# Kernel tuning notes

Hardware: AMD Instinct MI355X
Metric: run time of the kernel (lower is better)

The kernel has to match this reference:

```python
import jax, jax.numpy as jnp
import numpy as np

N_NODES = 100000
IN_CH, HID_CH, OUT_CH = 128, 128, 64
N_EDGES = 1600000


def _gcn_conv(x, W, b, src, dst, num_nodes):
    """PyG GCNConv with gcn_norm(add_self_loops=True): adds one self-loop per
    node to the given edge set, symmetric deg^-1/2 normalization, then
    gather-scale-scatter of the linearly transformed features."""
    loop = jnp.arange(num_nodes)
    s = jnp.concatenate([src, loop])
    d = jnp.concatenate([dst, loop])
    # degree over targets (flow source_to_target), edge weights = 1
    deg = jax.ops.segment_sum(jnp.ones_like(s, x.dtype), d, num_segments=num_nodes)
    dinv = jnp.where(deg > 0, deg ** -0.5, 0.0)
    norm = dinv[s] * dinv[d]                      # [E']
    h = x @ W                                     # [N, out]
    msg = h[s] * norm[:, None]                    # [E', out] gather + scale
    out = jax.ops.segment_sum(msg, d, num_segments=num_nodes)  # scatter-add
    return out + b


def setup_inputs() -> dict:
    key = jax.random.key(0)
    k = jax.random.split(key, 6)
    x = jax.random.normal(k[0], (N_NODES, IN_CH), dtype=jnp.float32)
    edge_index = jax.random.randint(k[1], (2, N_EDGES), 0, N_NODES, dtype=jnp.int64)
    # Glorot-scale params
    W1 = jax.random.normal(k[2], (IN_CH, HID_CH), dtype=jnp.float32) * (2.0 / (IN_CH + HID_CH)) ** 0.5
    b1 = jnp.zeros((HID_CH,), dtype=jnp.float32)
    W2 = jax.random.normal(k[3], (HID_CH, OUT_CH), dtype=jnp.float32) * (2.0 / (HID_CH + OUT_CH)) ** 0.5
    b2 = jnp.zeros((OUT_CH,), dtype=jnp.float32)
    return {"x": x, "edge_index": edge_index, "W1": W1, "b1": b1, "W2": W2, "b2": b2}


def reference(x, edge_index, W1, b1, W2, b2):
    num_nodes = x.shape[0]
    loop = jnp.arange(num_nodes, dtype=edge_index.dtype)
    # wrapper-level add_self_loops (GCNConv adds another internally)
    src = jnp.concatenate([edge_index[0], loop])
    dst = jnp.concatenate([edge_index[1], loop])
    h = _gcn_conv(x, W1, b1, src, dst, num_nodes)
    h = jax.nn.relu(h)
    h = _gcn_conv(h, W2, b2, src, dst, num_nodes)
    return jax.nn.log_softmax(h, axis=1)
```

## Files before the change

### kernel.cpp

```cpp
#include <hip/hip_runtime.h>
#include <cstdint>
#include <cstddef>

#define IN_CH 128
#define HID_CH 128
#define OUT_CH 64
#define BSH 8
#define PB 4096

typedef unsigned int uint32;
typedef unsigned char uchar;
typedef short bf16x8 __attribute__((ext_vector_type(8)));
typedef float f32x4 __attribute__((ext_vector_type(4)));
typedef float f32x2 __attribute__((ext_vector_type(2)));

static __device__ __forceinline__ unsigned short f2bf(float f) {
    uint32 u = __float_as_uint(f);
    u += 0x7fffu + ((u >> 16) & 1u);
    return (unsigned short)(u >> 16);
}
static __device__ __forceinline__ uchar f2fp8(float f) {
    int p = __builtin_amdgcn_cvt_pk_fp8_f32(f, f, 0, false);
    return (uchar)(p & 0xff);
}


__global__ __launch_bounds__(256) void bhist_wtrans(
    const int* __restrict__ dst, int* __restrict__ bcnt, int E, int NB, int gP,
    const float* __restrict__ W1, const float* __restrict__ W2,
    unsigned short* __restrict__ W1t, unsigned short* __restrict__ W2t) {
    if (blockIdx.x >= (uint32)gP) {
        int t = (blockIdx.x - gP) * 256 + threadIdx.x;
        if (t < 128 * 128) {
            int nc = t >> 7, k = t & 127;
            W1t[t] = f2bf(W1[k * 128 + nc]);
        }
        int u = t - 128 * 128;
        if (u >= 0 && u < 64 * 128) {
            int nc = u >> 7, k = u & 127;
            W2t[u] = f2bf(W2[k * 64 + nc]);
        }
        return;
    }
    __shared__ int h[512];
    int t = threadIdx.x;
    int e0 = blockIdx.x * PB;
    int cnt = min(PB, E - e0);
    for (int b = t; b < NB; b += 256) h[b] = 0;
    __syncthreads();
    for (int i = t; i < cnt; i += 256)
        atomicAdd(&h[dst[e0 + i] >> BSH], 1);
    __syncthreads();
    for (int b = t; b < NB; b += 256)
        if (h[b]) atomicAdd(&bcnt[b], h[b]);
}

__global__ void bscan(const int* __restrict__ bcnt, int* __restrict__ bbase,
                      int* __restrict__ bcur, int NB, int E) {
    __shared__ int s[512];
    int t = threadIdx.x;
    int v = (t < NB) ? bcnt[t] : 0;
    s[t] = v;
    __syncthreads();
    for (int o = 1; o < 512; o <<= 1) {
        int add = (t >= o) ? s[t - o] : 0;
        __syncthreads();
        s[t] += add;
        __syncthreads();
    }
    if (t < NB) { bbase[t] = s[t] - v; bcur[t] = 0; }
    if (t == 0) bbase[NB] = E;
}

__global__ __launch_bounds__(256) void part1(
    const int* __restrict__ src, const int* __restrict__ dst,
    const int* __restrict__ bbase, int* __restrict__ bcur,
    int2* __restrict__ pairBuf, int E, int NB) {
    __shared__ int2 pairs[PB];
    __shared__ int hist[512];
    __shared__ int base[512];
    int t = threadIdx.x;
    int e0 = blockIdx.x * PB;
    int cnt = min(PB, E - e0);
    for (int b = t; b < NB; b += 256) hist[b] = 0;
    __syncthreads();
    for (int i = t; i < cnt; i += 256) {
        int s = src[e0 + i], d = dst[e0 + i];
        pairs[i] = make_int2(s, d);
        atomicAdd(&hist[d >> BSH], 1);
    }
    __syncthreads();
    for (int b = t; b < NB; b += 256) {
        int h = hist[b];
        int gb = (h > 0) ? atomicAdd(&bcur[b], h) : 0;
        base[b] = bbase[b] + gb;
        hist[b] = 0;
    }
    __syncthreads();
    for (int i = t; i < cnt; i += 256) {
        int2 p = pairs[i];
        int b = p.y >> BSH;
        int q = base[b] + atomicAdd(&hist[b], 1);
        pairBuf[q] = p;
    }
}

__global__ __launch_bounds__(256) void bucket_build(
    const int2* __restrict__ pairBuf, const int* __restrict__ bbase,
    int* __restrict__ rowptr, int* __restrict__ deg, float* __restrict__ dinv,
    int* __restrict__ csr, int N) {
    __shared__ int cnt[256];
    __shared__ int loc[256];
    int b = blockIdx.x, t = threadIdx.x;
    int start = bbase[b], end = bbase[b + 1];
    cnt[t] = 0;
    __syncthreads();
    for (int i = start + t; i < end; i += 256)
        atomicAdd(&cnt[pairBuf[i].y & 255], 1);
    __syncthreads();
    int v = cnt[t];
    loc[t] = v;
    __syncthreads();
    for (int o = 1; o < 256; o <<= 1) {
        int add = (t >= o) ? loc[t - o] : 0;
        __syncthreads();
        loc[t] += add;
        __syncthreads();
    }
    int excl = loc[t] - v;
    int node = (b << BSH) + t;
    if (node < N) {
        rowptr[node] = start + excl;
        deg[node] = v;
        dinv[node] = rsqrtf((float)(v + 2));
    }
    __syncthreads();
    cnt[t] = excl;
    __syncthreads();
    for (int i = start + t; i < end; i += 256) {
        int2 p = pairBuf[i];
        int q = start + atomicAdd(&cnt[p.y & 255], 1);
        csr[q] = p.x;
    }
}


template <int OUT, bool AFP32>
__global__ __launch_bounds__(256) void gemm_mfma(
    const void* __restrict__ Av, const unsigned short* __restrict__ Wt,
    uchar* __restrict__ C, int n) {
    constexpr int AP = 72;
    constexpr int WP = 136;
    constexpr int NT = OUT / 16;
    __shared__ unsigned short As[128 * AP];
    __shared__ unsigned short Ws[OUT * WP];

    const int t = threadIdx.x;
    const int row0 = blockIdx.x * 128;

    for (int i = t; i < OUT * 16; i += 256) {
        int rr = i >> 4, sq = i & 15;
        *(uint4*)&Ws[rr * WP + sq * 8] = *(const uint4*)(Wt + rr * 128 + sq * 8);
    }

    const int w = t >> 6, l = t & 63;
    const int q = l >> 4, r16 = l & 15;
    const int mbase = w * 32;

    f32x4 acc0[NT], acc1[NT];
    for (int i = 0; i < NT; i++) {
        acc0[i] = (f32x4){0.f, 0.f, 0.f, 0.f};
        acc1[i] = (f32x4){0.f, 0.f, 0.f, 0.f};
    }

    for (int half = 0; half < 2; half++) {
        if (half) __syncthreads();
        if (AFP32) {
            const float* A = (const float*)Av;
            for (int i = t; i < 128 * 16; i += 256) {
                int rr = i >> 4, fq = i & 15;
                float4 v = make_float4(0.f, 0.f, 0.f, 0.f);
                if (row0 + rr < n)
                    v = *(const float4*)(A + (size_t)(row0 + rr) * 128 + half * 64 + fq * 4);
                unsigned short* p = &As[rr * AP + fq * 4];
                p[0] = f2bf(v.x); p[1] = f2bf(v.y); p[2] = f2bf(v.z); p[3] = f2bf(v.w);
            }
        } else {
            const unsigned short* A = (const unsigned short*)Av;
            for (int i = t; i < 128 * 8; i += 256) {
                int rr = i >> 3, sq = i & 7;
                uint4 v = make_uint4(0, 0, 0, 0);
                if (row0 + rr < n)
                    v = *(const uint4*)(A + (size_t)(row0 + rr) * 128 + half * 64 + sq * 8);
                *(uint4*)&As[rr * AP + sq * 8] = v;
            }
        }
        __syncthreads();

#pragma unroll
        for (int kc = 0; kc < 2; kc++) {
            int ko = kc * 32 + q * 8;
            int kow = half * 64 + ko;
            bf16x8 a0 = *(const bf16x8*)&As[(mbase + r16) * AP + ko];
            bf16x8 a1 = *(const bf16x8*)&As[(mbase + 16 + r16) * AP + ko];
#pragma unroll
            for (int nt = 0; nt < NT; nt++) {
                bf16x8 b = *(const bf16x8*)&Ws[(nt * 16 + r16) * WP + kow];
                acc0[nt] = __builtin_amdgcn_mfma_f32_16x16x32_bf16(a0, b, acc0[nt], 0, 0, 0);
                acc1[nt] = __builtin_amdgcn_mfma_f32_16x16x32_bf16(a1, b, acc1[nt], 0, 0, 0);
            }
        }
    }

#pragma unroll
    for (int nt = 0; nt < NT; nt++) {
#pragma unroll
        for (int p = 0; p < 4; p++) {
            int rr = row0 + mbase + q * 4 + p;
            if (rr < n) C[(size_t)rr * OUT + nt * 16 + r16] = f2fp8(acc0[nt][p]);
            if (rr + 16 < n) C[(size_t)(rr + 16) * OUT + nt * 16 + r16] = f2fp8(acc1[nt][p]);
        }
    }
}


__global__ __launch_bounds__(256) void agg_relu_128(
    const uchar* __restrict__ H, const int* __restrict__ csr,
    const int* __restrict__ rowptr, const int* __restrict__ deg,
    const float* __restrict__ dinv, const float* __restrict__ bias,
    unsigned short* __restrict__ out, int n) {
    int v = blockIdx.x * 16 + (threadIdx.x >> 4);
    int hl = threadIdx.x & 15;
    int gsel = threadIdx.x & 48;
    bool valid = v < n;
    int vc = valid ? v : 0;
    int base = rowptr[vc];
    int cnt = valid ? deg[vc] : 0;

    float4 aL0 = make_float4(0.f, 0.f, 0.f, 0.f), aH0 = aL0;
    float4 aL1 = aL0, aH1 = aL0, aL2 = aL0, aH2 = aL0, aL3 = aL0, aH3 = aL0;

    for (int j0 = 0; j0 < cnt; j0 += 16) {
        int nj = min(16, cnt - j0);
        int ul = 0; float wl = 0.f;
        if (hl < nj) { ul = csr[base + j0 + hl]; wl = dinv[ul]; }
        int j = 0;
        for (; j + 4 <= nj; j += 4) {
            int s0 = j | gsel, s1 = (j + 1) | gsel, s2 = (j + 2) | gsel, s3 = (j + 3) | gsel;
            int u0 = __shfl(ul, s0), u1 = __shfl(ul, s1);
            int u2 = __shfl(ul, s2), u3 = __shfl(ul, s3);
            float w0 = __shfl(wl, s0), w1 = __shfl(wl, s1);
            float w2 = __shfl(wl, s2), w3 = __shfl(wl, s3);
            uint2 h0 = *(const uint2*)(H + (size_t)u0 * 128 + hl * 8);
            uint2 h1 = *(const uint2*)(H + (size_t)u1 * 128 + hl * 8);
            uint2 h2 = *(const uint2*)(H + (size_t)u2 * 128 + hl * 8);
            uint2 h3 = *(const uint2*)(H + (size_t)u3 * 128 + hl * 8);
            {
                f32x2 p0 = __builtin_amdgcn_cvt_pk_f32_fp8(h0.x, false);
                f32x2 p1 = __builtin_amdgcn_cvt_pk_f32_fp8(h0.x, true);
                f32x2 p2 = __builtin_amdgcn_cvt_pk_f32_fp8(h0.y, false);
                f32x2 p3 = __builtin_amdgcn_cvt_pk_f32_fp8(h0.y, true);
                aL0.x += w0 * p0[0]; aL0.y += w0 * p0[1]; aL0.z += w0 * p1[0]; aL0.w += w0 * p1[1];
                aH0.x += w0 * p2[0]; aH0.y += w0 * p2[1]; aH0.z += w0 * p3[0]; aH0.w += w0 * p3[1];
            }
            {
                f32x2 p0 = __builtin_amdgcn_cvt_pk_f32_fp8(h1.x, false);
                f32x2 p1 = __builtin_amdgcn_cvt_pk_f32_fp8(h1.x, true);
                f32x2 p2 = __builtin_amdgcn_cvt_pk_f32_fp8(h1.y, false);
                f32x2 p3 = __builtin_amdgcn_cvt_pk_f32_fp8(h1.y, true);
                aL1.x += w1 * p0[0]; aL1.y += w1 * p0[1]; aL1.z += w1 * p1[0]; aL1.w += w1 * p1[1];
                aH1.x += w1 * p2[0]; aH1.y += w1 * p2[1]; aH1.z += w1 * p3[0]; aH1.w += w1 * p3[1];
            }
            {
                f32x2 p0 = __builtin_amdgcn_cvt_pk_f32_fp8(h2.x, false);
                f32x2 p1 = __builtin_amdgcn_cvt_pk_f32_fp8(h2.x, true);
                f32x2 p2 = __builtin_amdgcn_cvt_pk_f32_fp8(h2.y, false);
                f32x2 p3 = __builtin_amdgcn_cvt_pk_f32_fp8(h2.y, true);
                aL2.x += w2 * p0[0]; aL2.y += w2 * p0[1]; aL2.z += w2 * p1[0]; aL2.w += w2 * p1[1];
                aH2.x += w2 * p2[0]; aH2.y += w2 * p2[1]; aH2.z += w2 * p3[0]; aH2.w += w2 * p3[1];
            }
            {
                f32x2 p0 = __builtin_amdgcn_cvt_pk_f32_fp8(h3.x, false);
                f32x2 p1 = __builtin_amdgcn_cvt_pk_f32_fp8(h3.x, true);
                f32x2 p2 = __builtin_amdgcn_cvt_pk_f32_fp8(h3.y, false);
                f32x2 p3 = __builtin_amdgcn_cvt_pk_f32_fp8(h3.y, true);
                aL3.x += w3 * p0[0]; aL3.y += w3 * p0[1]; aL3.z += w3 * p1[0]; aL3.w += w3 * p1[1];
                aH3.x += w3 * p2[0]; aH3.y += w3 * p2[1]; aH3.z += w3 * p3[0]; aH3.w += w3 * p3[1];
            }
        }
        for (; j < nj; j++) {
            int s = j | gsel;
            int u = __shfl(ul, s);
            float wv = __shfl(wl, s);
            uint2 h = *(const uint2*)(H + (size_t)u * 128 + hl * 8);
            f32x2 p0 = __builtin_amdgcn_cvt_pk_f32_fp8(h.x, false);
            f32x2 p1 = __builtin_amdgcn_cvt_pk_f32_fp8(h.x, true);
            f32x2 p2 = __builtin_amdgcn_cvt_pk_f32_fp8(h.y, false);
            f32x2 p3 = __builtin_amdgcn_cvt_pk_f32_fp8(h.y, true);
            aL0.x += wv * p0[0]; aL0.y += wv * p0[1]; aL0.z += wv * p1[0]; aL0.w += wv * p1[1];
            aH0.x += wv * p2[0]; aH0.y += wv * p2[1]; aH0.z += wv * p3[0]; aH0.w += wv * p3[1];
        }
    }
    if (valid) {
        float4 aL = make_float4((aL0.x + aL1.x) + (aL2.x + aL3.x),
                                (aL0.y + aL1.y) + (aL2.y + aL3.y),
                                (aL0.z + aL1.z) + (aL2.z + aL3.z),
                                (aL0.w + aL1.w) + (aL2.w + aL3.w));
        float4 aH = make_float4((aH0.x + aH1.x) + (aH2.x + aH3.x),
                                (aH0.y + aH1.y) + (aH2.y + aH3.y),
                                (aH0.z + aH1.z) + (aH2.z + aH3.z),
                                (aH0.w + aH1.w) + (aH2.w + aH3.w));
        float dv = dinv[vc];
        float sl = 2.f * dv * dv;
        uint2 hv = *(const uint2*)(H + (size_t)vc * 128 + hl * 8);
        f32x2 s0 = __builtin_amdgcn_cvt_pk_f32_fp8(hv.x, false);
        f32x2 s1 = __builtin_amdgcn_cvt_pk_f32_fp8(hv.x, true);
        f32x2 s2 = __builtin_amdgcn_cvt_pk_f32_fp8(hv.y, false);
        f32x2 s3 = __builtin_amdgcn_cvt_pk_f32_fp8(hv.y, true);
        const float4* bp = (const float4*)(bias + hl * 8);
        float4 b0 = bp[0], b1 = bp[1];
        float o0 = fmaxf(dv * aL.x + sl * s0[0] + b0.x, 0.f);
        float o1 = fmaxf(dv * aL.y + sl * s0[1] + b0.y, 0.f);
        float o2 = fmaxf(dv * aL.z + sl * s1[0] + b0.z, 0.f);
        float o3 = fmaxf(dv * aL.w + sl * s1[1] + b0.w, 0.f);
        float o4 = fmaxf(dv * aH.x + sl * s2[0] + b1.x, 0.f);
        float o5 = fmaxf(dv * aH.y + sl * s2[1] + b1.y, 0.f);
        float o6 = fmaxf(dv * aH.z + sl * s3[0] + b1.z, 0.f);
        float o7 = fmaxf(dv * aH.w + sl * s3[1] + b1.w, 0.f);
        uint4 pk;
        pk.x = (uint32)f2bf(o0) | ((uint32)f2bf(o1) << 16);
        pk.y = (uint32)f2bf(o2) | ((uint32)f2bf(o3) << 16);
        pk.z = (uint32)f2bf(o4) | ((uint32)f2bf(o5) << 16);
        pk.w = (uint32)f2bf(o6) | ((uint32)f2bf(o7) << 16);
        *(uint4*)(out + (size_t)vc * 128 + hl * 8) = pk;
    }
}

__global__ __launch_bounds__(256) void agg_lsm_64(
    const uchar* __restrict__ H, const int* __restrict__ csr,
    const int* __restrict__ rowptr, const int* __restrict__ deg,
    const float* __restrict__ dinv, const float* __restrict__ bias,
    float* __restrict__ out, int n) {
    int v = blockIdx.x * 16 + (threadIdx.x >> 4);
    int hl = threadIdx.x & 15;
    int gsel = threadIdx.x & 48;
    bool valid = v < n;
    int vc = valid ? v : 0;
    int base = rowptr[vc];
    int cnt = valid ? deg[vc] : 0;

    float4 a0 = make_float4(0.f, 0.f, 0.f, 0.f), a1 = a0, a2 = a0, a3 = a0;
    for (int j0 = 0; j0 < cnt; j0 += 16) {
        int nj = min(16, cnt - j0);
        int ul = 0; float wl = 0.f;
        if (hl < nj) { ul = csr[base + j0 + hl]; wl = dinv[ul]; }
        int j = 0;
        for (; j + 4 <= nj; j += 4) {
            int s0 = j | gsel, s1 = (j + 1) | gsel, s2 = (j + 2) | gsel, s3 = (j + 3) | gsel;
            int u0 = __shfl(ul, s0), u1 = __shfl(ul, s1);
            int u2 = __shfl(ul, s2), u3 = __shfl(ul, s3);
            float w0 = __shfl(wl, s0), w1 = __shfl(wl, s1);
            float w2 = __shfl(wl, s2), w3 = __shfl(wl, s3);
            uint32 h0 = *(const uint32*)(H + (size_t)u0 * 64 + hl * 4);
            uint32 h1 = *(const uint32*)(H + (size_t)u1 * 64 + hl * 4);
            uint32 h2 = *(const uint32*)(H + (size_t)u2 * 64 + hl * 4);
            uint32 h3 = *(const uint32*)(H + (size_t)u3 * 64 + hl * 4);
            f32x2 l0 = __builtin_amdgcn_cvt_pk_f32_fp8(h0, false);
            f32x2 g0 = __builtin_amdgcn_cvt_pk_f32_fp8(h0, true);
            f32x2 l1 = __builtin_amdgcn_cvt_pk_f32_fp8(h1, false);
            f32x2 g1 = __builtin_amdgcn_cvt_pk_f32_fp8(h1, true);
            f32x2 l2 = __builtin_amdgcn_cvt_pk_f32_fp8(h2, false);
            f32x2 g2 = __builtin_amdgcn_cvt_pk_f32_fp8(h2, true);
            f32x2 l3 = __builtin_amdgcn_cvt_pk_f32_fp8(h3, false);
            f32x2 g3 = __builtin_amdgcn_cvt_pk_f32_fp8(h3, true);
            a0.x += w0 * l0[0]; a0.y += w0 * l0[1]; a0.z += w0 * g0[0]; a0.w += w0 * g0[1];
            a1.x += w1 * l1[0]; a1.y += w1 * l1[1]; a1.z += w1 * g1[0]; a1.w += w1 * g1[1];
            a2.x += w2 * l2[0]; a2.y += w2 * l2[1]; a2.z += w2 * g2[0]; a2.w += w2 * g2[1];
            a3.x += w3 * l3[0]; a3.y += w3 * l3[1]; a3.z += w3 * g3[0]; a3.w += w3 * g3[1];
        }
        for (; j < nj; j++) {
            int s = j | gsel;
            int u = __shfl(ul, s);
            float wv = __shfl(wl, s);
            uint32 h = *(const uint32*)(H + (size_t)u * 64 + hl * 4);
            f32x2 lo = __builtin_amdgcn_cvt_pk_f32_fp8(h, false);
            f32x2 gg = __builtin_amdgcn_cvt_pk_f32_fp8(h, true);
            a0.x += wv * lo[0]; a0.y += wv * lo[1]; a0.z += wv * gg[0]; a0.w += wv * gg[1];
        }
    }
    float4 acc = make_float4((a0.x + a1.x) + (a2.x + a3.x),
                             (a0.y + a1.y) + (a2.y + a3.y),
                             (a0.z + a1.z) + (a2.z + a3.z),
                             (a0.w + a1.w) + (a2.w + a3.w));
    float dv = dinv[vc];
    uint32 hv = *(const uint32*)(H + (size_t)vc * 64 + hl * 4);
    f32x2 dl = __builtin_amdgcn_cvt_pk_f32_fp8(hv, false);
    f32x2 dh = __builtin_amdgcn_cvt_pk_f32_fp8(hv, true);
    float4 bb = ((const float4*)bias)[hl];
    float sl = 2.f * dv * dv;
    float v0 = dv * acc.x + sl * dl[0] + bb.x;
    float v1 = dv * acc.y + sl * dl[1] + bb.y;
    float v2 = dv * acc.z + sl * dh[0] + bb.z;
    float v3 = dv * acc.w + sl * dh[1] + bb.w;
    float m = fmaxf(fmaxf(v0, v1), fmaxf(v2, v3));
    for (int o = 8; o > 0; o >>= 1) m = fmaxf(m, __shfl_xor(m, o));
    float e = (__expf(v0 - m) + __expf(v1 - m)) + (__expf(v2 - m) + __expf(v3 - m));
    for (int o = 8; o > 0; o >>= 1) e += __shfl_xor(e, o);
    float ls = m + __logf(e);
    if (valid)
        *(float4*)(out + (size_t)vc * 64 + hl * 4) =
            make_float4(v0 - ls, v1 - ls, v2 - ls, v3 - ls);
}


extern "C" void kernel_launch(void* const* d_in, const int* in_sizes, int n_in,
                              void* d_out, int out_size, void* d_ws, size_t ws_size,
                              hipStream_t stream) {
    const float* x  = (const float*)d_in[0];
    const int*   ei = (const int*)d_in[1];
    const float* W1 = (const float*)d_in[2];
    const float* b1 = (const float*)d_in[3];
    const float* W2 = (const float*)d_in[4];
    const float* b2 = (const float*)d_in[5];
    float* out = (float*)d_out;

    const int N = in_sizes[0] / IN_CH;
    const int E = in_sizes[1] / 2;
    const int* src = ei;
    const int* dst = ei + E;
    const int NB = (N + 255) >> BSH;

    char* w = (char*)d_ws;
    size_t off = 0;
    auto alloc = [&](size_t bytes) -> char* {
        char* p = w + off;
        off = (off + bytes + 255) & ~(size_t)255;
        return p;
    };
    int*   deg    = (int*)alloc((size_t)N * 4);
    int*   rowptr = (int*)alloc((size_t)N * 4);
    int*   bcnt   = (int*)alloc(512 * 4);
    int*   bbase  = (int*)alloc(513 * 4);
    int*   bcur   = (int*)alloc(512 * 4);
    float* dinv   = (float*)alloc((size_t)N * 4);
    int*   csr    = (int*)alloc((size_t)E * 4);
    unsigned short* W1t = (unsigned short*)alloc(128 * 128 * 2);
    unsigned short* W2t = (unsigned short*)alloc(64 * 128 * 2);
    uchar* H1  = (uchar*)alloc((size_t)N * HID_CH);
    unsigned short* A1b = (unsigned short*)alloc((size_t)N * HID_CH * 2);
    uchar* H2  = H1;
    int2*  pairBuf = (int2*)A1b;

    hipMemsetAsync(bcnt, 0, 512 * 4, stream);

    int gP = (E + PB - 1) / PB;

    bhist_wtrans<<<gP + 96, 256, 0, stream>>>(dst, bcnt, E, NB, gP, W1, W2, W1t, W2t);
    bscan<<<1, 512, 0, stream>>>(bcnt, bbase, bcur, NB, E);
    part1<<<gP, 256, 0, stream>>>(src, dst, bbase, bcur, pairBuf, E, NB);
    bucket_build<<<NB, 256, 0, stream>>>(pairBuf, bbase, rowptr, deg, dinv, csr, N);

    gemm_mfma<128, true><<<(N + 127) / 128, 256, 0, stream>>>(x, W1t, H1, N);
    agg_relu_128<<<(N + 15) / 16, 256, 0, stream>>>(H1, csr, rowptr, deg, dinv, b1, A1b, N);
    gemm_mfma<64, false><<<(N + 127) / 128, 256, 0, stream>>>(A1b, W2t, H2, N);
    agg_lsm_64<<<(N + 15) / 16, 256, 0, stream>>>(H2, csr, rowptr, deg, dinv, b2, out, N);
}
```

Baseline: 252.9 us.

## Fuse edge partition with first GEMM and vectorize aggregation accumulators

Merges the edge-partition kernel and the first MFMA GEMM into one launch, where the first blocks do the partition and the later blocks do GEMM tiles. The two independent phases can then run concurrently, and one launch plus a serialization point are removed. The shared memory is unioned at 53 KB, which may lower occupancy for the partition blocks. The aggregation kernels also switch to packed f32x2 accumulators, aiming for packed FMA instructions.

Result: no change. 253.0 us (+0.1%).

```diff
diff --git a/kernel.cpp b/kernel.cpp
--- a/kernel.cpp
+++ b/kernel.cpp
@@ -72,91 +72,15 @@
     if (t == 0) bbase[NB] = E;
 }
 
-__global__ __launch_bounds__(256) void part1(
-    const int* __restrict__ src, const int* __restrict__ dst,
-    const int* __restrict__ bbase, int* __restrict__ bcur,
-    int2* __restrict__ pairBuf, int E, int NB) {
-    __shared__ int2 pairs[PB];
-    __shared__ int hist[512];
-    __shared__ int base[512];
-    int t = threadIdx.x;
-    int e0 = blockIdx.x * PB;
-    int cnt = min(PB, E - e0);
-    for (int b = t; b < NB; b += 256) hist[b] = 0;
-    __syncthreads();
-    for (int i = t; i < cnt; i += 256) {
-        int s = src[e0 + i], d = dst[e0 + i];
-        pairs[i] = make_int2(s, d);
-        atomicAdd(&hist[d >> BSH], 1);
-    }
-    __syncthreads();
-    for (int b = t; b < NB; b += 256) {
-        int h = hist[b];
-        int gb = (h > 0) ? atomicAdd(&bcur[b], h) : 0;
-        base[b] = bbase[b] + gb;
-        hist[b] = 0;
-    }
-    __syncthreads();
-    for (int i = t; i < cnt; i += 256) {
-        int2 p = pairs[i];
-        int b = p.y >> BSH;
-        int q = base[b] + atomicAdd(&hist[b], 1);
-        pairBuf[q] = p;
-    }
-}
-
-__global__ __launch_bounds__(256) void bucket_build(
-    const int2* __restrict__ pairBuf, const int* __restrict__ bbase,
-    int* __restrict__ rowptr, int* __restrict__ deg, float* __restrict__ dinv,
-    int* __restrict__ csr, int N) {
-    __shared__ int cnt[256];
-    __shared__ int loc[256];
-    int b = blockIdx.x, t = threadIdx.x;
-    int start = bbase[b], end = bbase[b + 1];
-    cnt[t] = 0;
-    __syncthreads();
-    for (int i = start + t; i < end; i += 256)
-        atomicAdd(&cnt[pairBuf[i].y & 255], 1);
-    __syncthreads();
-    int v = cnt[t];
-    loc[t] = v;
-    __syncthreads();
-    for (int o = 1; o < 256; o <<= 1) {
-        int add = (t >= o) ? loc[t - o] : 0;
-        __syncthreads();
-        loc[t] += add;
-        __syncthreads();
-    }
-    int excl = loc[t] - v;
-    int node = (b << BSH) + t;
-    if (node < N) {
-        rowptr[node] = start + excl;
-        deg[node] = v;
-        dinv[node] = rsqrtf((float)(v + 2));
-    }
-    __syncthreads();
-    cnt[t] = excl;
-    __syncthreads();
-    for (int i = start + t; i < end; i += 256) {
-        int2 p = pairBuf[i];
-        int q = start + atomicAdd(&cnt[p.y & 255], 1);
-        csr[q] = p.x;
-    }
-}
-
 
 template <int OUT, bool AFP32>
-__global__ __launch_bounds__(256) void gemm_mfma(
+static __device__ __forceinline__ void gemm_body(
+    unsigned short* As, unsigned short* Ws,
     const void* __restrict__ Av, const unsigned short* __restrict__ Wt,
-    uchar* __restrict__ C, int n) {
+    uchar* __restrict__ C, int n, int row0, int t) {
     constexpr int AP = 72;
     constexpr int WP = 136;
     constexpr int NT = OUT / 16;
-    __shared__ unsigned short As[128 * AP];
-    __shared__ unsigned short Ws[OUT * WP];
-
-    const int t = threadIdx.x;
-    const int row0 = blockIdx.x * 128;
 
     for (int i = t; i < OUT * 16; i += 256) {
         int rr = i >> 4, sq = i & 15;
@@ -223,6 +147,98 @@
     }
 }
 
+__global__ __launch_bounds__(256) void part1_gemm1(
+    const int* __restrict__ src, const int* __restrict__ dst,
+    const int* __restrict__ bbase, int* __restrict__ bcur,
+    int2* __restrict__ pairBuf, int E, int NB, int gP,
+    const float* __restrict__ x, const unsigned short* __restrict__ W1t,
+    uchar* __restrict__ H1, int n) {
+    __shared__ __align__(16) char smem[53248];
+    int t = threadIdx.x;
+
+    if ((int)blockIdx.x >= gP) {
+        unsigned short* As = (unsigned short*)smem;
+        unsigned short* Ws = (unsigned short*)(smem + 18432);
+        gemm_body<128, true>(As, Ws, x, W1t, H1, n, ((int)blockIdx.x - gP) * 128, t);
+        return;
+    }
+
+    int2* pairs = (int2*)smem;
+    int*  hist  = (int*)(smem + 32768);
+    int*  base  = (int*)(smem + 32768 + 2048);
+    int e0 = blockIdx.x * PB;
+    int cnt = min(PB, E - e0);
+    for (int b = t; b < NB; b += 256) hist[b] = 0;
+    __syncthreads();
+    for (int i = t; i < cnt; i += 256) {
+        int s = src[e0 + i], d = dst[e0 + i];
+        pairs[i] = make_int2(s, d);
+        atomicAdd(&hist[d >> BSH], 1);
+    }
+    __syncthreads();
+    for (int b = t; b < NB; b += 256) {
+        int h = hist[b];
+        int gb = (h > 0) ? atomicAdd(&bcur[b], h) : 0;
+        base[b] = bbase[b] + gb;
+        hist[b] = 0;
+    }
+    __syncthreads();
+    for (int i = t; i < cnt; i += 256) {
+        int2 p = pairs[i];
+        int b = p.y >> BSH;
+        int q = base[b] + atomicAdd(&hist[b], 1);
+        pairBuf[q] = p;
+    }
+}
+
+__global__ __launch_bounds__(256) void bucket_build(
+    const int2* __restrict__ pairBuf, const int* __restrict__ bbase,
+    int* __restrict__ rowptr, int* __restrict__ deg, float* __restrict__ dinv,
+    int* __restrict__ csr, int N) {
+    __shared__ int cnt[256];
+    __shared__ int loc[256];
+    int b = blockIdx.x, t = threadIdx.x;
+    int start = bbase[b], end = bbase[b + 1];
+    cnt[t] = 0;
+    __syncthreads();
+    for (int i = start + t; i < end; i += 256)
+        atomicAdd(&cnt[pairBuf[i].y & 255], 1);
+    __syncthreads();
+    int v = cnt[t];
+    loc[t] = v;
+    __syncthreads();
+    for (int o = 1; o < 256; o <<= 1) {
+        int add = (t >= o) ? loc[t - o] : 0;
+        __syncthreads();
+        loc[t] += add;
+        __syncthreads();
+    }
+    int excl = loc[t] - v;
+    int node = (b << BSH) + t;
+    if (node < N) {
+        rowptr[node] = start + excl;
+        deg[node] = v;
+        dinv[node] = rsqrtf((float)(v + 2));
+    }
+    __syncthreads();
+    cnt[t] = excl;
+    __syncthreads();
+    for (int i = start + t; i < end; i += 256) {
+        int2 p = pairBuf[i];
+        int q = start + atomicAdd(&cnt[p.y & 255], 1);
+        csr[q] = p.x;
+    }
+}
+
+template <int OUT, bool AFP32>
+__global__ __launch_bounds__(256) void gemm_mfma(
+    const void* __restrict__ Av, const unsigned short* __restrict__ Wt,
+    uchar* __restrict__ C, int n) {
+    __shared__ unsigned short As[128 * 72];
+    __shared__ unsigned short Ws[OUT * 136];
+    gemm_body<OUT, AFP32>(As, Ws, Av, Wt, C, n, blockIdx.x * 128, threadIdx.x);
+}
+
 
 __global__ __launch_bounds__(256) void agg_relu_128(
     const uchar* __restrict__ H, const int* __restrict__ csr,
@@ -237,8 +253,11 @@
     int base = rowptr[vc];
     int cnt = valid ? deg[vc] : 0;
 
-    float4 aL0 = make_float4(0.f, 0.f, 0.f, 0.f), aH0 = aL0;
-    float4 aL1 = aL0, aH1 = aL0, aL2 = aL0, aH2 = aL0, aL3 = aL0, aH3 = aL0;
+    f32x2 acc[4][4];
+#pragma unroll
+    for (int i = 0; i < 4; i++)
+#pragma unroll
+        for (int p = 0; p < 4; p++) acc[i][p] = (f32x2){0.f, 0.f};
 
     for (int j0 = 0; j0 < cnt; j0 += 16) {
         int nj = min(16, cnt - j0);
@@ -255,61 +274,45 @@
             uint2 h1 = *(const uint2*)(H + (size_t)u1 * 128 + hl * 8);
             uint2 h2 = *(const uint2*)(H + (size_t)u2 * 128 + hl * 8);
             uint2 h3 = *(const uint2*)(H + (size_t)u3 * 128 + hl * 8);
-            {
-                f32x2 p0 = __builtin_amdgcn_cvt_pk_f32_fp8(h0.x, false);
-                f32x2 p1 = __builtin_amdgcn_cvt_pk_f32_fp8(h0.x, true);
-                f32x2 p2 = __builtin_amdgcn_cvt_pk_f32_fp8(h0.y, false);
-                f32x2 p3 = __builtin_amdgcn_cvt_pk_f32_fp8(h0.y, true);
-                aL0.x += w0 * p0[0]; aL0.y += w0 * p0[1]; aL0.z += w0 * p1[0]; aL0.w += w0 * p1[1];
-                aH0.x += w0 * p2[0]; aH0.y += w0 * p2[1]; aH0.z += w0 * p3[0]; aH0.w += w0 * p3[1];
-            }
-            {
-                f32x2 p0 = __builtin_amdgcn_cvt_pk_f32_fp8(h1.x, false);
-                f32x2 p1 = __builtin_amdgcn_cvt_pk_f32_fp8(h1.x, true);
-                f32x2 p2 = __builtin_amdgcn_cvt_pk_f32_fp8(h1.y, false);
-                f32x2 p3 = __builtin_amdgcn_cvt_pk_f32_fp8(h1.y, true);
-                aL1.x += w1 * p0[0]; aL1.y += w1 * p0[1]; aL1.z += w1 * p1[0]; aL1.w += w1 * p1[1];
-                aH1.x += w1 * p2[0]; aH1.y += w1 * p2[1]; aH1.z += w1 * p3[0]; aH1.w += w1 * p3[1];
-            }
-            {
-                f32x2 p0 = __builtin_amdgcn_cvt_pk_f32_fp8(h2.x, false);
-                f32x2 p1 = __builtin_amdgcn_cvt_pk_f32_fp8(h2.x, true);
-                f32x2 p2 = __builtin_amdgcn_cvt_pk_f32_fp8(h2.y, false);
-                f32x2 p3 = __builtin_amdgcn_cvt_pk_f32_fp8(h2.y, true);
-                aL2.x += w2 * p0[0]; aL2.y += w2 * p0[1]; aL2.z += w2 * p1[0]; aL2.w += w2 * p1[1];
-                aH2.x += w2 * p2[0]; aH2.y += w2 * p2[1]; aH2.z += w2 * p3[0]; aH2.w += w2 * p3[1];
-            }
-            {
-                f32x2 p0 = __builtin_amdgcn_cvt_pk_f32_fp8(h3.x, false);
-                f32x2 p1 = __builtin_amdgcn_cvt_pk_f32_fp8(h3.x, true);
-                f32x2 p2 = __builtin_amdgcn_cvt_pk_f32_fp8(h3.y, false);
-                f32x2 p3 = __builtin_amdgcn_cvt_pk_f32_fp8(h3.y, true);
-                aL3.x += w3 * p0[0]; aL3.y += w3 * p0[1]; aL3.z += w3 * p1[0]; aL3.w += w3 * p1[1];
-                aH3.x += w3 * p2[0]; aH3.y += w3 * p2[1]; aH3.z += w3 * p3[0]; aH3.w += w3 * p3[1];
-            }
+            f32x2 wv;
+            wv = (f32x2){w0, w0};
+            acc[0][0] += wv * __builtin_amdgcn_cvt_pk_f32_fp8(h0.x, false);
+            acc[0][1] += wv * __builtin_amdgcn_cvt_pk_f32_fp8(h0.x, true);
+            acc[0][2] += wv * __builtin_amdgcn_cvt_pk_f32_fp8(h0.y, false);
+            acc[0][3] += wv * __builtin_amdgcn_cvt_pk_f32_fp8(h0.y, true);
+            wv = (f32x2){w1, w1};
+            acc[1][0] += wv * __builtin_amdgcn_cvt_pk_f32_fp8(h1.x, false);
+            acc[1][1] += wv * __builtin_amdgcn_cvt_pk_f32_fp8(h1.x, true);
+            acc[1][2] += wv * __builtin_amdgcn_cvt_pk_f32_fp8(h1.y, false);
+            acc[1][3] += wv * __builtin_amdgcn_cvt_pk_f32_fp8(h1.y, true);
+            wv = (f32x2){w2, w2};
+            acc[2][0] += wv * __builtin_amdgcn_cvt_pk_f32_fp8(h2.x, false);
+            acc[2][1] += wv * __builtin_amdgcn_cvt_pk_f32_fp8(h2.x, true);
+            acc[2][2] += wv * __builtin_amdgcn_cvt_pk_f32_fp8(h2.y, false);
+            acc[2][3] += wv * __builtin_amdgcn_cvt_pk_f32_fp8(h2.y, true);
+            wv = (f32x2){w3, w3};
+            acc[3][0] += wv * __builtin_amdgcn_cvt_pk_f32_fp8(h3.x, false);
+            acc[3][1] += wv * __builtin_amdgcn_cvt_pk_f32_fp8(h3.x, true);
+            acc[3][2] += wv * __builtin_amdgcn_cvt_pk_f32_fp8(h3.y, false);
+            acc[3][3] += wv * __builtin_amdgcn_cvt_pk_f32_fp8(h3.y, true);
         }
         for (; j < nj; j++) {
             int s = j | gsel;
             int u = __shfl(ul, s);
-            float wv = __shfl(wl, s);
+            float wf = __shfl(wl, s);
             uint2 h = *(const uint2*)(H + (size_t)u * 128 + hl * 8);
-            f32x2 p0 = __builtin_amdgcn_cvt_pk_f32_fp8(h.x, false);
-            f32x2 p1 = __builtin_amdgcn_cvt_pk_f32_fp8(h.x, true);
-            f32x2 p2 = __builtin_amdgcn_cvt_pk_f32_fp8(h.y, false);
-            f32x2 p3 = __builtin_amdgcn_cvt_pk_f32_fp8(h.y, true);
-            aL0.x += wv * p0[0]; aL0.y += wv * p0[1]; aL0.z += wv * p1[0]; aL0.w += wv * p1[1];
-            aH0.x += wv * p2[0]; aH0.y += wv * p2[1]; aH0.z += wv * p3[0]; aH0.w += wv * p3[1];
+            f32x2 wv = (f32x2){wf, wf};
+            acc[0][0] += wv * __builtin_amdgcn_cvt_pk_f32_fp8(h.x, false);
+            acc[0][1] += wv * __builtin_amdgcn_cvt_pk_f32_fp8(h.x, true);
+            acc[0][2] += wv * __builtin_amdgcn_cvt_pk_f32_fp8(h.y, false);
+            acc[0][3] += wv * __builtin_amdgcn_cvt_pk_f32_fp8(h.y, true);
         }
     }
     if (valid) {
-        float4 aL = make_float4((aL0.x + aL1.x) + (aL2.x + aL3.x),
-                                (aL0.y + aL1.y) + (aL2.y + aL3.y),
-                                (aL0.z + aL1.z) + (aL2.z + aL3.z),
-                                (aL0.w + aL1.w) + (aL2.w + aL3.w));
-        float4 aH = make_float4((aH0.x + aH1.x) + (aH2.x + aH3.x),
-                                (aH0.y + aH1.y) + (aH2.y + aH3.y),
-                                (aH0.z + aH1.z) + (aH2.z + aH3.z),
-                                (aH0.w + aH1.w) + (aH2.w + aH3.w));
+        f32x2 a0 = (acc[0][0] + acc[1][0]) + (acc[2][0] + acc[3][0]);
+        f32x2 a1 = (acc[0][1] + acc[1][1]) + (acc[2][1] + acc[3][1]);
+        f32x2 a2 = (acc[0][2] + acc[1][2]) + (acc[2][2] + acc[3][2]);
+        f32x2 a3 = (acc[0][3] + acc[1][3]) + (acc[2][3] + acc[3][3]);
         float dv = dinv[vc];
         float sl = 2.f * dv * dv;
         uint2 hv = *(const uint2*)(H + (size_t)vc * 128 + hl * 8);
@@ -319,14 +322,14 @@
         f32x2 s3 = __builtin_amdgcn_cvt_pk_f32_fp8(hv.y, true);
         const float4* bp = (const float4*)(bias + hl * 8);
         float4 b0 = bp[0], b1 = bp[1];
-        float o0 = fmaxf(dv * aL.x + sl * s0[0] + b0.x, 0.f);
-        float o1 = fmaxf(dv * aL.y + sl * s0[1] + b0.y, 0.f);
-        float o2 = fmaxf(dv * aL.z + sl * s1[0] + b0.z, 0.f);
-        float o3 = fmaxf(dv * aL.w + sl * s1[1] + b0.w, 0.f);
-        float o4 = fmaxf(dv * aH.x + sl * s2[0] + b1.x, 0.f);
-        float o5 = fmaxf(dv * aH.y + sl * s2[1] + b1.y, 0.f);
-        float o6 = fmaxf(dv * aH.z + sl * s3[0] + b1.z, 0.f);
-        float o7 = fmaxf(dv * aH.w + sl * s3[1] + b1.w, 0.f);
+        float o0 = fmaxf(dv * a0[0] + sl * s0[0] + b0.x, 0.f);
+        float o1 = fmaxf(dv * a0[1] + sl * s0[1] + b0.y, 0.f);
+        float o2 = fmaxf(dv * a1[0] + sl * s1[0] + b0.z, 0.f);
+        float o3 = fmaxf(dv * a1[1] + sl * s1[1] + b0.w, 0.f);
+        float o4 = fmaxf(dv * a2[0] + sl * s2[0] + b1.x, 0.f);
+        float o5 = fmaxf(dv * a2[1] + sl * s2[1] + b1.y, 0.f);
+        float o6 = fmaxf(dv * a3[0] + sl * s3[0] + b1.z, 0.f);
+        float o7 = fmaxf(dv * a3[1] + sl * s3[1] + b1.w, 0.f);
         uint4 pk;
         pk.x = (uint32)f2bf(o0) | ((uint32)f2bf(o1) << 16);
         pk.y = (uint32)f2bf(o2) | ((uint32)f2bf(o3) << 16);
@@ -349,7 +352,13 @@
     int base = rowptr[vc];
     int cnt = valid ? deg[vc] : 0;
 
-    float4 a0 = make_float4(0.f, 0.f, 0.f, 0.f), a1 = a0, a2 = a0, a3 = a0;
+    f32x2 acc[4][2];
+#pragma unroll
+    for (int i = 0; i < 4; i++) {
+        acc[i][0] = (f32x2){0.f, 0.f};
+        acc[i][1] = (f32x2){0.f, 0.f};
+    }
+
     for (int j0 = 0; j0 < cnt; j0 += 16) {
         int nj = min(16, cnt - j0);
         int ul = 0; float wl = 0.f;
@@ -365,43 +374,42 @@
             uint32 h1 = *(const uint32*)(H + (size_t)u1 * 64 + hl * 4);
             uint32 h2 = *(const uint32*)(H + (size_t)u2 * 64 + hl * 4);
             uint32 h3 = *(const uint32*)(H + (size_t)u3 * 64 + hl * 4);
-            f32x2 l0 = __builtin_amdgcn_cvt_pk_f32_fp8(h0, false);
-            f32x2 g0 = __builtin_amdgcn_cvt_pk_f32_fp8(h0, true);
-            f32x2 l1 = __builtin_amdgcn_cvt_pk_f32_fp8(h1, false);
-            f32x2 g1 = __builtin_amdgcn_cvt_pk_f32_fp8(h1, true);
-            f32x2 l2 = __builtin_amdgcn_cvt_pk_f32_fp8(h2, false);
-            f32x2 g2 = __builtin_amdgcn_cvt_pk_f32_fp8(h2, true);
-            f32x2 l3 = __builtin_amdgcn_cvt_pk_f32_fp8(h3, false);
-            f32x2 g3 = __builtin_amdgcn_cvt_pk_f32_fp8(h3, true);
-            a0.x += w0 * l0[0]; a0.y += w0 * l0[1]; a0.z += w0 * g0[0]; a0.w += w0 * g0[1];
-            a1.x += w1 * l1[0]; a1.y += w1 * l1[1]; a1.z += w1 * g1[0]; a1.w += w1 * g1[1];
-            a2.x += w2 * l2[0]; a2.y += w2 * l2[1]; a2.z += w2 * g2[0]; a2.w += w2 * g2[1];
-            a3.x += w3 * l3[0]; a3.y += w3 * l3[1]; a3.z += w3 * g3[0]; a3.w += w3 * g3[1];
+            f32x2 wv;
+            wv = (f32x2){w0, w0};
+            acc[0][0] += wv * __builtin_amdgcn_cvt_pk_f32_fp8(h0, false);
+            acc[0][1] += wv * __builtin_amdgcn_cvt_pk_f32_fp8(h0, true);
+            wv = (f32x2){w1, w1};
+            acc[1][0] += wv * __builtin_amdgcn_cvt_pk_f32_fp8(h1, false);
+            acc[1][1] += wv * __builtin_amdgcn_cvt_pk_f32_fp8(h1, true);
+            wv = (f32x2){w2, w2};
+            acc[2][0] += wv * __builtin_amdgcn_cvt_pk_f32_fp8(h2, false);
+            acc[2][1] += wv * __builtin_amdgcn_cvt_pk_f32_fp8(h2, true);
+            wv = (f32x2){w3, w3};
+            acc[3][0] += wv * __builtin_amdgcn_cvt_pk_f32_fp8(h3, false);
+            acc[3][1] += wv * __builtin_amdgcn_cvt_pk_f32_fp8(h3, true);
         }
         for (; j < nj; j++) {
             int s = j | gsel;
             int u = __shfl(ul, s);
-            float wv = __shfl(wl, s);
+            float wf = __shfl(wl, s);
             uint32 h = *(const uint32*)(H + (size_t)u * 64 + hl * 4);
-            f32x2 lo = __builtin_amdgcn_cvt_pk_f32_fp8(h, false);
-            f32x2 gg = __builtin_amdgcn_cvt_pk_f32_fp8(h, true);
-            a0.x += wv * lo[0]; a0.y += wv * lo[1]; a0.z += wv * gg[0]; a0.w += wv * gg[1];
-        }
-    }
-    float4 acc = make_float4((a0.x + a1.x) + (a2.x + a3.x),
-                             (a0.y + a1.y) + (a2.y + a3.y),
-                             (a0.z + a1.z) + (a2.z + a3.z),
-                             (a0.w + a1.w) + (a2.w + a3.w));
+            f32x2 wv = (f32x2){wf, wf};
+            acc[0][0] += wv * __builtin_amdgcn_cvt_pk_f32_fp8(h, false);
+            acc[0][1] += wv * __builtin_amdgcn_cvt_pk_f32_fp8(h, true);
+        }
+    }
+    f32x2 aL = (acc[0][0] + acc[1][0]) + (acc[2][0] + acc[3][0]);
+    f32x2 aH = (acc[0][1] + acc[1][1]) + (acc[2][1] + acc[3][1]);
     float dv = dinv[vc];
     uint32 hv = *(const uint32*)(H + (size_t)vc * 64 + hl * 4);
     f32x2 dl = __builtin_amdgcn_cvt_pk_f32_fp8(hv, false);
     f32x2 dh = __builtin_amdgcn_cvt_pk_f32_fp8(hv, true);
     float4 bb = ((const float4*)bias)[hl];
     float sl = 2.f * dv * dv;
-    float v0 = dv * acc.x + sl * dl[0] + bb.x;
-    float v1 = dv * acc.y + sl * dl[1] + bb.y;
-    float v2 = dv * acc.z + sl * dh[0] + bb.z;
-    float v3 = dv * acc.w + sl * dh[1] + bb.w;
+    float v0 = dv * aL[0] + sl * dl[0] + bb.x;
+    float v1 = dv * aL[1] + sl * dl[1] + bb.y;
+    float v2 = dv * aH[0] + sl * dh[0] + bb.z;
+    float v3 = dv * aH[1] + sl * dh[1] + bb.w;
     float m = fmaxf(fmaxf(v0, v1), fmaxf(v2, v3));
     for (int o = 8; o > 0; o >>= 1) m = fmaxf(m, __shfl_xor(m, o));
     float e = (__expf(v0 - m) + __expf(v1 - m)) + (__expf(v2 - m) + __expf(v3 - m));
@@ -454,13 +462,14 @@
     hipMemsetAsync(bcnt, 0, 512 * 4, stream);
 
     int gP = (E + PB - 1) / PB;
+    int gG1 = (N + 127) / 128;
 
     bhist_wtrans<<<gP + 96, 256, 0, stream>>>(dst, bcnt, E, NB, gP, W1, W2, W1t, W2t);
     bscan<<<1, 512, 0, stream>>>(bcnt, bbase, bcur, NB, E);
-    part1<<<gP, 256, 0, stream>>>(src, dst, bbase, bcur, pairBuf, E, NB);
+    part1_gemm1<<<gP + gG1, 256, 0, stream>>>(src, dst, bbase, bcur, pairBuf, E, NB, gP,
+                                              x, W1t, H1, N);
     bucket_build<<<NB, 256, 0, stream>>>(pairBuf, bbase, rowptr, deg, dinv, csr, N);
 
-    gemm_mfma<128, true><<<(N + 127) / 128, 256, 0, stream>>>(x, W1t, H1, N);
     agg_relu_128<<<(N + 15) / 16, 256, 0, stream>>>(H1, csr, rowptr, deg, dinv, b1, A1b, N);
     gemm_mfma<64, false><<<(N + 127) / 128, 256, 0, stream>>>(A1b, W2t, H2, N);
     agg_lsm_64<<<(N + 15) / 16, 256, 0, stream>>>(H2, csr, rowptr, deg, dinv, b2, out, N);
```
